# Optimization experiments

Hardware: AMD Instinct MI355X
Metric: run time of the kernel (lower is better)

Reference implementation:

```python
import jax, jax.numpy as jnp
import numpy as np

N_NODES = 50000
N_EDGES = 800000
NEG_SLOPE = 0.2


def _gat_conv(h, src, dst, W, al, ar, b, res, act):
    """DGL-style GATConv. h:[N,Fin], W:[Fin,H*D], al/ar:[H,D], b:[H*D].
    res: None | [N,H,D] residual value. Returns [N,H,D]."""
    N = h.shape[0]
    H, D = al.shape
    ft = (h @ W).reshape(N, H, D)                       # projected features
    el = jnp.einsum('nhd,hd->nh', ft, al)               # [N,H]
    er = jnp.einsum('nhd,hd->nh', ft, ar)               # [N,H]
    e = jax.nn.leaky_relu(el[src] + er[dst], NEG_SLOPE) # [E,H] edge logits
    # edge softmax over incoming edges of each dst node
    emax = jax.ops.segment_max(e, dst, num_segments=N)  # [N,H]
    emax = jnp.where(jnp.isfinite(emax), emax, 0.0)     # guard empty segments
    ex = jnp.exp(e - emax[dst])                         # [E,H]
    denom = jax.ops.segment_sum(ex, dst, num_segments=N)
    a = ex / denom[dst]                                 # [E,H] attention
    rst = jax.ops.segment_sum(ft[src] * a[..., None], dst, num_segments=N)  # [N,H,D]
    if res is not None:
        rst = rst + res
    rst = rst + b.reshape(1, H, D)
    if act is not None:
        rst = act(rst)
    return rst


def setup_inputs() -> dict:
    key = jax.random.key(0)
    ks = jax.random.split(key, 16)
    s = 0.1
    return {
        'x': jax.random.normal(ks[0], (N_NODES, 128), jnp.float32),
        'edge_src': jax.random.randint(ks[1], (N_EDGES,), 0, N_NODES, jnp.int32),
        'edge_dst': jax.random.randint(ks[2], (N_EDGES,), 0, N_NODES, jnp.int32),
        'W0': jax.random.normal(ks[3], (128, 128), jnp.float32) * s,
        'al0': jax.random.normal(ks[4], (2, 64), jnp.float32) * s,
        'ar0': jax.random.normal(ks[5], (2, 64), jnp.float32) * s,
        'b0': jnp.zeros((128,), jnp.float32),
        'W1': jax.random.normal(ks[6], (128, 128), jnp.float32) * s,
        'al1': jax.random.normal(ks[7], (2, 64), jnp.float32) * s,
        'ar1': jax.random.normal(ks[8], (2, 64), jnp.float32) * s,
        'b1': jnp.zeros((128,), jnp.float32),
        'W2': jax.random.normal(ks[9], (128, 194), jnp.float32) * s,
        'al2': jax.random.normal(ks[10], (2, 97), jnp.float32) * s,
        'ar2': jax.random.normal(ks[11], (2, 97), jnp.float32) * s,
        'b2': jnp.zeros((194,), jnp.float32),
        'res_W2': jax.random.normal(ks[12], (128, 194), jnp.float32) * s,
    }


def reference(x, edge_src, edge_dst, W0, al0, ar0, b0, W1, al1, ar1, b1,
              W2, al2, ar2, b2, res_W2):
    N = x.shape[0]
    elu = jax.nn.elu
    # layer 0: no residual, ELU
    h = _gat_conv(x, edge_src, edge_dst, W0, al0, ar0, b0, None, elu)
    h = h.reshape(N, -1)                                # flatten(1) -> [N,128]
    # layer 1: identity residual (in == heads*out), ELU
    res1 = h.reshape(N, 2, 64)
    h = _gat_conv(h, edge_src, edge_dst, W1, al1, ar1, b1, res1, elu)
    h = h.reshape(N, -1)
    # output layer: linear residual, no activation, mean over heads
    res2 = (h @ res_W2).reshape(N, 2, 97)
    logits = _gat_conv(h, edge_src, edge_dst, W2, al2, ar2, b2, res2, None)
    logits = logits.mean(axis=1)                        # [N, 97]
    # original slices off the last node of each graph (single batched graph)
    return logits[: N - 1]
```

## Files before the change

### kernel.cpp

```cpp
#include <hip/hip_runtime.h>
#include <math.h>

#define NNODES 50000
#define NEDGES 800000
#define NPAD   50048
#define NSLICE 8
#define SLICEN (NNODES / NSLICE)

typedef unsigned int uint;
typedef unsigned short u16;
typedef __bf16 bf16x8 __attribute__((ext_vector_type(8)));
typedef float f32x4 __attribute__((ext_vector_type(4)));

__device__ __forceinline__ float lrelu(float x){ return x > 0.f ? x : 0.2f*x; }
__device__ __forceinline__ float elu_f(float x){ return x > 0.f ? x : expm1f(x); }
__device__ __forceinline__ u16 f2bf(float f){
    uint u = __float_as_uint(f);
    return (u16)((u + 0x7fffu + ((u >> 16) & 1u)) >> 16);
}
__device__ __forceinline__ float bf2f(u16 h){ return __uint_as_float(((uint)h) << 16); }
__device__ __forceinline__ float blo(uint u){ return __uint_as_float(u << 16); }
__device__ __forceinline__ float bhi(uint u){ return __uint_as_float(u & 0xffff0000u); }

#define R0 (NPAD*32)
#define R1 (R0 + 256*128)
#define R2 (R1 + 128*384)
#define R3 (R2 + 256)
#define R4 (R3 + 128)
__global__ void prep_all(const float* __restrict__ x,
                         const float* __restrict__ W0, const float* __restrict__ W1,
                         const float* __restrict__ W2, const float* __restrict__ Wr,
                         const float* __restrict__ al2, const float* __restrict__ ar2,
                         const float* __restrict__ b2,
                         u16* __restrict__ Xb, u16* __restrict__ H1b,
                         u16* __restrict__ B01, u16* __restrict__ Bf,
                         float* __restrict__ alp2, float* __restrict__ arp2,
                         float* __restrict__ cb, int N)
{
    int idx = blockIdx.x * blockDim.x + threadIdx.x;
    if (idx < R0) {
        int n = idx >> 5;
        ushort4 hv = make_ushort4(0,0,0,0);
        if (n < N) {
            float4 v = ((const float4*)x)[idx];
            hv.x = f2bf(v.x); hv.y = f2bf(v.y); hv.z = f2bf(v.z); hv.w = f2bf(v.w);
        } else {
            ((ushort4*)H1b)[idx] = make_ushort4(0,0,0,0);
        }
        ((ushort4*)Xb)[idx] = hv;
    } else if (idx < R1) {
        int j = idx - R0, gcol = j >> 7, k = j & 127;
        float v = (gcol < 128) ? W0[k*128 + gcol] : W1[k*128 + (gcol - 128)];
        B01[j] = f2bf(v);
    } else if (idx < R2) {
        int j = idx - R1, c = j / 384, k = j - c*384;
        float v = 0.f;
        if (c < 97) {
            if (k < 128)      v = W2[k*194 + c];
            else if (k < 256) v = W2[(k-128)*194 + 97 + c];
            else              v = Wr[(k-256)*194 + c] + Wr[(k-256)*194 + 97 + c];
        }
        Bf[c*384 + k] = f2bf(v);
    } else if (idx < R3) {
        int t = idx - R2, k = t & 127, h = t >> 7;
        float sl = 0.f, sr = 0.f;
        for (int d = 0; d < 97; d++) {
            float w = W2[k*194 + h*97 + d];
            sl += w * al2[h*97 + d];
            sr += w * ar2[h*97 + d];
        }
        alp2[h*128 + k] = sl;
        arp2[h*128 + k] = sr;
    } else if (idx < R4) {
        int c = idx - R3;
        if (c < 97) cb[c] = 0.5f * (b2[c] + b2[97 + c]);
    }
}

__global__ __launch_bounds__(256, 4)
void gemm_l01(const u16* __restrict__ Ab, const u16* __restrict__ Bh, u16* __restrict__ obf,
              const float* __restrict__ alv, const float* __restrict__ arv,
              float* __restrict__ el, float* __restrict__ er, int N)
{
    __shared__ u16 sB[128 * 136];
    const int bm = blockIdx.x * 64;
    const int tid = threadIdx.x, wid = tid >> 6, lane = tid & 63;
    const int lr = lane & 15, q = lane >> 4, lk8 = q << 3;

    bf16x8 aH[4];
    {
        size_t abase = (size_t)(bm + wid*16 + lr) * 128 + lk8;
        #pragma unroll
        for (int kt = 0; kt < 4; kt++)
            aH[kt] = *(const bf16x8*)(Ab + abase + kt*32);
    }
    {
        const int c = tid >> 1, seg = (tid & 1) * 64;
        const u16* g = Bh + (size_t)c * 128 + seg;
        u16* s = sB + c * 136 + seg;
        #pragma unroll
        for (int j = 0; j < 8; j++)
            *(uint4*)(s + j*8) = *(const uint4*)(g + j*8);
    }
    __syncthreads();

    f32x4 acc[8];
    #pragma unroll
    for (int i = 0; i < 8; i++) acc[i] = (f32x4){0.f,0.f,0.f,0.f};

    #pragma unroll
    for (int kt = 0; kt < 4; kt++)
        #pragma unroll
        for (int fs = 0; fs < 8; fs++) {
            bf16x8 b = *(const bf16x8*)(sB + (fs*16 + lr)*136 + kt*32 + lk8);
            acc[fs] = __builtin_amdgcn_mfma_f32_16x16x32_bf16(aH[kt], b, acc[fs], 0, 0, 0);
        }

    float el0[4] = {0,0,0,0}, el1[4] = {0,0,0,0}, er0[4] = {0,0,0,0}, er1[4] = {0,0,0,0};
    #pragma unroll
    for (int fs = 0; fs < 8; fs++) {
        const int col = fs*16 + lr;
        const float av = alv[col], gv = arv[col];
        #pragma unroll
        for (int v = 0; v < 4; v++) {
            float f = acc[fs][v];
            int row = bm + wid*16 + q*4 + v;
            if (row < N) obf[(size_t)row * 128 + col] = f2bf(f);
            if (fs < 4) { el0[v] += f * av; er0[v] += f * gv; }
            else        { el1[v] += f * av; er1[v] += f * gv; }
        }
    }
    #pragma unroll
    for (int off = 1; off < 16; off <<= 1) {
        #pragma unroll
        for (int v = 0; v < 4; v++) {
            el0[v] += __shfl_xor(el0[v], off);
            el1[v] += __shfl_xor(el1[v], off);
            er0[v] += __shfl_xor(er0[v], off);
            er1[v] += __shfl_xor(er1[v], off);
        }
    }
    if (lr == 0) {
        #pragma unroll
        for (int v = 0; v < 4; v++) {
            int row = bm + wid*16 + q*4 + v;
            if (row < N) {
                *(float2*)(el + 2*(size_t)row) = make_float2(el0[v], el1[v]);
                *(float2*)(er + 2*(size_t)row) = make_float2(er0[v], er1[v]);
            }
        }
    }
}

__global__ __launch_bounds__(256, 3)
void gemm_final(const u16* __restrict__ agg01, const u16* __restrict__ h2b,
                const u16* __restrict__ Bf, const float* __restrict__ cb,
                float* __restrict__ out, int N)
{
    __shared__ u16 sB[64 * 392];
    const int bid = blockIdx.x;
    const int x = (bid >> 4) * 8 + (bid & 7);
    const int ct = (bid >> 3) & 1;
    if (x >= NPAD / 64) return;
    const int bm = x * 64;
    const int tid = threadIdx.x, wid = tid >> 6, lane = tid & 63;
    const int lr = lane & 15, q = lane >> 4, lk8 = q << 3;

    bf16x8 aF[12];
    {
        const int row = bm + wid*16 + lr;
        const u16* pa = agg01 + (size_t)row * 256;
        #pragma unroll
        for (int kt = 0; kt < 8; kt++)
            aF[kt] = *(const bf16x8*)(pa + kt*32 + lk8);
        const u16* ph = h2b + (size_t)row * 128;
        #pragma unroll
        for (int kt = 0; kt < 4; kt++)
            aF[8 + kt] = *(const bf16x8*)(ph + kt*32 + lk8);
    }
    {
        const int c = tid >> 2, seg = (tid & 3) * 96;
        const u16* g = Bf + (size_t)(ct*64 + c) * 384 + seg;
        u16* s = sB + c * 392 + seg;
        #pragma unroll
        for (int j = 0; j < 12; j++)
            *(uint4*)(s + j*8) = *(const uint4*)(g + j*8);
    }
    __syncthreads();

    f32x4 acc[4];
    #pragma unroll
    for (int i = 0; i < 4; i++) acc[i] = (f32x4){0.f,0.f,0.f,0.f};

    #pragma unroll
    for (int kt = 0; kt < 12; kt++)
        #pragma unroll
        for (int fs = 0; fs < 4; fs++) {
            bf16x8 b = *(const bf16x8*)(sB + (fs*16 + lr)*392 + kt*32 + lk8);
            acc[fs] = __builtin_amdgcn_mfma_f32_16x16x32_bf16(aF[kt], b, acc[fs], 0, 0, 0);
        }

    #pragma unroll
    for (int fs = 0; fs < 4; fs++) {
        const int col = ct*64 + fs*16 + lr;
        if (col >= 97) continue;
        const float cbc = cb[col];
        #pragma unroll
        for (int v = 0; v < 4; v++) {
            int row = bm + wid*16 + q*4 + v;
            if (row < N - 1) out[(size_t)row * 97 + col] = 0.5f * acc[fs][v] + cbc;
        }
    }
}

__global__ __launch_bounds__(256)
void hist_sliced(const int* __restrict__ dst, int* __restrict__ counts, int E)
{
    const int slice = blockIdx.x & (NSLICE - 1);
    const int lo = slice * SLICEN, hi = lo + SLICEN;
    const int stride = (gridDim.x >> 3) * blockDim.x;
    for (int i = (blockIdx.x >> 3) * blockDim.x + threadIdx.x; i < E; i += stride) {
        int d = dst[i];
        if (d >= lo && d < hi) atomicAdd(&counts[d], 1);
    }
}

__global__ __launch_bounds__(256)
void scatter_sliced(const int* __restrict__ src, const int* __restrict__ dst,
                    int* __restrict__ cursor, int* __restrict__ ssorted, int E)
{
    const int slice = blockIdx.x & (NSLICE - 1);
    const int lo = slice * SLICEN, hi = lo + SLICEN;
    const int stride = (gridDim.x >> 3) * blockDim.x;
    for (int i = (blockIdx.x >> 3) * blockDim.x + threadIdx.x; i < E; i += stride) {
        int d = dst[i];
        if (d >= lo && d < hi) {
            int p = atomicAdd(&cursor[d], 1);
            ssorted[p] = src[i];
        }
    }
}

__global__ __launch_bounds__(1024)
void scan_dl(int* __restrict__ cnt_cur, int* __restrict__ row_start,
             int* __restrict__ flags, int* __restrict__ prefixes, int n)
{
    __shared__ int wsum[16];
    __shared__ int sExc;
    const int tid = threadIdx.x, lane = tid & 63, wv = tid >> 6;
    const int i0 = blockIdx.x * 4096 + tid * 4;
    int c[4], v[4];
    #pragma unroll
    for (int j = 0; j < 4; j++) { int i = i0 + j; c[j] = (i < n) ? cnt_cur[i] : 0; }
    v[0] = c[0]; v[1] = v[0] + c[1]; v[2] = v[1] + c[2]; v[3] = v[2] + c[3];
    int t = v[3];
    #pragma unroll
    for (int off = 1; off < 64; off <<= 1) {
        int u = __shfl_up(t, off);
        if (lane >= off) t += u;
    }
    int texcl = t - v[3];
    if (lane == 63) wsum[wv] = t;
    __syncthreads();
    if (tid == 0) {
        int tot = 0;
        #pragma unroll
        for (int w = 0; w < 16; w++) tot += wsum[w];
        int exc = 0;
        if (blockIdx.x > 0) {
            while (atomicAdd(&flags[blockIdx.x - 1], 0) == 0) __builtin_amdgcn_s_sleep(2);
            exc = atomicAdd(&prefixes[blockIdx.x - 1], 0);
        } else {
            row_start[0] = 0;
        }
        atomicExch(&prefixes[blockIdx.x], exc + tot);
        __threadfence();
        atomicExch(&flags[blockIdx.x], 1);
        sExc = exc;
    }
    __syncthreads();
    int woff = sExc + texcl;
    for (int w = 0; w < 16; w++) if (w < wv) woff += wsum[w];
    #pragma unroll
    for (int j = 0; j < 4; j++) {
        int i = i0 + j;
        if (i < n) {
            int inc = woff + v[j];
            row_start[i + 1] = inc;
            cnt_cur[i] = inc - c[j];
        }
    }
}

template<int MODE>
__global__ __launch_bounds__(256)
void gat_agg128(const uint* __restrict__ ftb, const float* __restrict__ el,
                const float* __restrict__ er, const int* __restrict__ row_start,
                const int* __restrict__ ssorted, const u16* __restrict__ Rb,
                const float* __restrict__ bias, u16* __restrict__ Hb,
                const float* __restrict__ alp2, const float* __restrict__ arp2,
                float* __restrict__ el2, float* __restrict__ er2)
{
    __shared__ int   s_src[4][64];
    __shared__ float s_w[4][2][64];
    const int wv = threadIdx.x >> 6, lane = threadIdx.x & 63;
    const int n = blockIdx.x * 4 + wv;
    const int beg = row_start[n];
    const int deg = row_start[n+1] - beg;
    const float2 ern = *(const float2*)(er + 2*(size_t)n);
    const int h = lane >> 5;
    float ax = 0.f, ay = 0.f, dp0 = 0.f, dp1 = 0.f;

    for (int cb = 0; cb < deg; cb += 64) {
        const int cnt = min(64, deg - cb);
        float w0 = 0.f, w1 = 0.f; int s = 0;
        if (lane < cnt) {
            s = ssorted[beg + cb + lane];
            float2 e = *(const float2*)(el + 2*(size_t)s);
            w0 = __expf(lrelu(e.x + ern.x));
            w1 = __expf(lrelu(e.y + ern.y));
        }
        dp0 += w0; dp1 += w1;
        s_src[wv][lane] = s; s_w[wv][0][lane] = w0; s_w[wv][1][lane] = w1;
        asm volatile("s_waitcnt lgkmcnt(0)" ::: "memory");
        int t = 0;
        for (; t + 8 <= cnt; t += 8) {
            int4   sa = *(const int4*)&s_src[wv][t];
            int4   sb = *(const int4*)&s_src[wv][t+4];
            float4 wa = *(const float4*)&s_w[wv][h][t];
            float4 wb = *(const float4*)&s_w[wv][h][t+4];
            int   sv[8] = {sa.x,sa.y,sa.z,sa.w,sb.x,sb.y,sb.z,sb.w};
            float wj[8] = {wa.x,wa.y,wa.z,wa.w,wb.x,wb.y,wb.z,wb.w};
            uint U[8];
            #pragma unroll
            for (int j = 0; j < 8; j++) U[j] = ftb[((uint)sv[j] << 6) + lane];
            #pragma unroll
            for (int j = 0; j < 8; j++) { ax += wj[j]*blo(U[j]); ay += wj[j]*bhi(U[j]); }
        }
        for (; t < cnt; t++) {
            int sv = s_src[wv][t];
            float w = s_w[wv][h][t];
            uint u = ftb[((uint)sv << 6) + lane];
            ax += w*blo(u); ay += w*bhi(u);
        }
    }
    #pragma unroll
    for (int off = 32; off; off >>= 1) { dp0 += __shfl_xor(dp0, off); dp1 += __shfl_xor(dp1, off); }
    const float den = (h == 0) ? dp0 : dp1;
    float r0 = (deg > 0) ? ax / den : 0.f;
    float r1 = (deg > 0) ? ay / den : 0.f;
    const int c0 = 2 * lane;
    const size_t ob = (size_t)n*128 + c0;
    const float2 bv = *(const float2*)(bias + c0);
    float v0 = r0 + bv.x, v1 = r1 + bv.y;
    if (MODE == 1) {
        ushort2 rv = *(const ushort2*)&Rb[ob];
        v0 += bf2f(rv.x);
        v1 += bf2f(rv.y);
    }
    v0 = elu_f(v0); v1 = elu_f(v1);
    *(ushort2*)&Hb[ob] = make_ushort2(f2bf(v0), f2bf(v1));

    if constexpr (MODE == 1) {
        float2 a0 = *(const float2*)(alp2 + c0);
        float2 a1 = *(const float2*)(alp2 + 128 + c0);
        float2 g0 = *(const float2*)(arp2 + c0);
        float2 g1 = *(const float2*)(arp2 + 128 + c0);
        float e0 = v0*a0.x + v1*a0.y;
        float e1 = v0*a1.x + v1*a1.y;
        float f0 = v0*g0.x + v1*g0.y;
        float f1 = v0*g1.x + v1*g1.y;
        #pragma unroll
        for (int off = 32; off; off >>= 1) {
            e0 += __shfl_xor(e0, off); e1 += __shfl_xor(e1, off);
            f0 += __shfl_xor(f0, off); f1 += __shfl_xor(f1, off);
        }
        if (lane == 0) {
            *(float2*)(el2 + 2*(size_t)n) = make_float2(e0, e1);
            *(float2*)(er2 + 2*(size_t)n) = make_float2(f0, f1);
        }
    }
}

__global__ __launch_bounds__(256)
void gat_agg_out2(const uint* __restrict__ h2u, const float* __restrict__ el,
                  const float* __restrict__ er, const int* __restrict__ row_start,
                  const int* __restrict__ ssorted, u16* __restrict__ agg01)
{
    __shared__ int   s_src[4][64];
    __shared__ float s_w[4][2][64];
    const int wv = threadIdx.x >> 6, lane = threadIdx.x & 63;
    const int n = blockIdx.x * 4 + wv;
    const int beg = row_start[n];
    const int deg = row_start[n+1] - beg;
    const float2 ern = *(const float2*)(er + 2*(size_t)n);
    float ax0 = 0.f, ay0 = 0.f, ax1 = 0.f, ay1 = 0.f, dp0 = 0.f, dp1 = 0.f;

    for (int cb = 0; cb < deg; cb += 64) {
        const int cnt = min(64, deg - cb);
        float w0 = 0.f, w1 = 0.f; int s = 0;
        if (lane < cnt) {
            s = ssorted[beg + cb + lane];
            float2 e = *(const float2*)(el + 2*(size_t)s);
            w0 = __expf(lrelu(e.x + ern.x));
            w1 = __expf(lrelu(e.y + ern.y));
        }
        dp0 += w0; dp1 += w1;
        s_src[wv][lane] = s; s_w[wv][0][lane] = w0; s_w[wv][1][lane] = w1;
        asm volatile("s_waitcnt lgkmcnt(0)" ::: "memory");
        int t = 0;
        for (; t + 8 <= cnt; t += 8) {
            int4   sa = *(const int4*)&s_src[wv][t];
            int4   sb = *(const int4*)&s_src[wv][t+4];
            float4 p0a = *(const float4*)&s_w[wv][0][t];
            float4 p0b = *(const float4*)&s_w[wv][0][t+4];
            float4 p1a = *(const float4*)&s_w[wv][1][t];
            float4 p1b = *(const float4*)&s_w[wv][1][t+4];
            int   sv[8] = {sa.x,sa.y,sa.z,sa.w,sb.x,sb.y,sb.z,sb.w};
            float f0[8] = {p0a.x,p0a.y,p0a.z,p0a.w,p0b.x,p0b.y,p0b.z,p0b.w};
            float f1[8] = {p1a.x,p1a.y,p1a.z,p1a.w,p1b.x,p1b.y,p1b.z,p1b.w};
            uint U[8];
            #pragma unroll
            for (int j = 0; j < 8; j++) U[j] = h2u[((uint)sv[j] << 6) + lane];
            #pragma unroll
            for (int j = 0; j < 8; j++) {
                float lo = blo(U[j]), hi = bhi(U[j]);
                ax0 += f0[j]*lo; ay0 += f0[j]*hi;
                ax1 += f1[j]*lo; ay1 += f1[j]*hi;
            }
        }
        for (; t < cnt; t++) {
            int sv = s_src[wv][t];
            float f0 = s_w[wv][0][t], f1 = s_w[wv][1][t];
            uint u = h2u[((uint)sv << 6) + lane];
            float lo = blo(u), hi = bhi(u);
            ax0 += f0*lo; ay0 += f0*hi;
            ax1 += f1*lo; ay1 += f1*hi;
        }
    }
    #pragma unroll
    for (int off = 32; off; off >>= 1) { dp0 += __shfl_xor(dp0, off); dp1 += __shfl_xor(dp1, off); }
    const float i0 = (deg > 0) ? 1.f/dp0 : 0.f;
    const float i1 = (deg > 0) ? 1.f/dp1 : 0.f;
    const int c0 = 2 * lane;
    *(ushort2*)&agg01[(size_t)n*256 + c0]       = make_ushort2(f2bf(ax0*i0), f2bf(ay0*i0));
    *(ushort2*)&agg01[(size_t)n*256 + 128 + c0] = make_ushort2(f2bf(ax1*i1), f2bf(ay1*i1));
}

extern "C" void kernel_launch(void* const* d_in, const int* in_sizes, int n_in,
                              void* d_out, int out_size, void* d_ws, size_t ws_size,
                              hipStream_t stream)
{
    const float* x   = (const float*)d_in[0];
    const int*   esrc= (const int*)  d_in[1];
    const int*   edst= (const int*)  d_in[2];
    const float* W0  = (const float*)d_in[3];
    const float* al0 = (const float*)d_in[4];
    const float* ar0 = (const float*)d_in[5];
    const float* b0  = (const float*)d_in[6];
    const float* W1  = (const float*)d_in[7];
    const float* al1 = (const float*)d_in[8];
    const float* ar1 = (const float*)d_in[9];
    const float* b1  = (const float*)d_in[10];
    const float* W2  = (const float*)d_in[11];
    const float* al2 = (const float*)d_in[12];
    const float* ar2 = (const float*)d_in[13];
    const float* b2  = (const float*)d_in[14];
    const float* rW2 = (const float*)d_in[15];
    float* out = (float*)d_out;

    const int N = NNODES, E = NEDGES;
    const int NB = (N + 4095) / 4096;
    float* ws = (float*)d_ws;
    size_t o = 0;
    auto alloc_f = [&](size_t count) { float* p = ws + o; o += (count + 3) & ~(size_t)3; return p; };
    float* el    = alloc_f((size_t)N * 2);
    float* er    = alloc_f((size_t)N * 2);
    float* el2   = alloc_f((size_t)N * 2);
    float* er2   = alloc_f((size_t)N * 2);
    uint*  ftb   = (uint*)alloc_f((size_t)N * 64);
    u16*   agg01 = (u16*)alloc_f((size_t)NPAD * 128);
    u16*   Xb    = (u16*)alloc_f((size_t)NPAD * 64);
    u16*   H1b   = (u16*)alloc_f((size_t)NPAD * 64);
    u16*   B01   = (u16*)alloc_f(256 * 64);
    u16*   Bf    = (u16*)alloc_f(128 * 192);
    float* alp2  = alloc_f(256);
    float* arp2  = alloc_f(256);
    float* cbv   = alloc_f(128);
    int* row_start = (int*)alloc_f(N + 4);
    int* cursor    = (int*)alloc_f(N + 64);
    int* flags     = cursor + N;
    int* prefixes  = cursor + N + 16;
    int* ssorted   = (int*)alloc_f(E);

    hipMemsetAsync(cursor, 0, (N + 64) * sizeof(int), stream);
    hist_sliced<<<NSLICE * 256, 256, 0, stream>>>(edst, cursor, E);
    scan_dl<<<NB, 1024, 0, stream>>>(cursor, row_start, flags, prefixes, N);
    scatter_sliced<<<NSLICE * 256, 256, 0, stream>>>(esrc, edst, cursor, ssorted, E);

    prep_all<<<(R4 + 255) / 256, 256, 0, stream>>>(x, W0, W1, W2, rW2, al2, ar2, b2,
                                                   Xb, H1b, B01, Bf, alp2, arp2, cbv, N);

    const int gx = NPAD / 64;
    const int agg_grid = N / 4;

    gemm_l01<<<gx, 256, 0, stream>>>(Xb, B01, (u16*)ftb, al0, ar0, el, er, N);
    gat_agg128<0><<<agg_grid, 256, 0, stream>>>(ftb, el, er, row_start, ssorted,
                                                nullptr, b0, H1b, nullptr, nullptr, nullptr, nullptr);

    gemm_l01<<<gx, 256, 0, stream>>>(H1b, B01 + 128*128, (u16*)ftb, al1, ar1, el, er, N);
    gat_agg128<1><<<agg_grid, 256, 0, stream>>>(ftb, el, er, row_start, ssorted,
                                                H1b, b1, Xb, alp2, arp2, el2, er2);

    gat_agg_out2<<<agg_grid, 256, 0, stream>>>((uint*)Xb, el2, er2, row_start, ssorted, agg01);
    gemm_final<<<((gx + 7) / 8) * 16, 256, 0, stream>>>(agg01, Xb, Bf, cbv, out, N);
}
```

Baseline: 281.2 us.

## Vectorize GAT neighbor gathers with 16-byte loads and merge prep with histogram

```diff
diff --git a/kernel.cpp b/kernel.cpp
--- a/kernel.cpp
+++ b/kernel.cpp
@@ -27,17 +27,32 @@
 #define R2 (R1 + 128*384)
 #define R3 (R2 + 256)
 #define R4 (R3 + 128)
-__global__ void prep_all(const float* __restrict__ x,
-                         const float* __restrict__ W0, const float* __restrict__ W1,
-                         const float* __restrict__ W2, const float* __restrict__ Wr,
-                         const float* __restrict__ al2, const float* __restrict__ ar2,
-                         const float* __restrict__ b2,
-                         u16* __restrict__ Xb, u16* __restrict__ H1b,
-                         u16* __restrict__ B01, u16* __restrict__ Bf,
-                         float* __restrict__ alp2, float* __restrict__ arp2,
-                         float* __restrict__ cb, int N)
-{
-    int idx = blockIdx.x * blockDim.x + threadIdx.x;
+#define PREPB ((R4 + 255) / 256)
+#define HISTB 2048
+__global__ __launch_bounds__(256)
+void prep_hist(const float* __restrict__ x,
+               const float* __restrict__ W0, const float* __restrict__ W1,
+               const float* __restrict__ W2, const float* __restrict__ Wr,
+               const float* __restrict__ al2, const float* __restrict__ ar2,
+               const float* __restrict__ b2,
+               const int* __restrict__ edst, int* __restrict__ counts,
+               u16* __restrict__ Xb, u16* __restrict__ H1b,
+               u16* __restrict__ B01, u16* __restrict__ Bf,
+               float* __restrict__ alp2, float* __restrict__ arp2,
+               float* __restrict__ cb, int N)
+{
+    if (blockIdx.x >= PREPB) {
+        const int hb = blockIdx.x - PREPB;
+        const int slice = hb & (NSLICE - 1);
+        const int lo = slice * SLICEN, hi = lo + SLICEN;
+        const int stride = (HISTB >> 3) * 256;
+        for (int i = (hb >> 3) * 256 + (int)threadIdx.x; i < NEDGES; i += stride) {
+            int d = edst[i];
+            if (d >= lo && d < hi) atomicAdd(&counts[d], 1);
+        }
+        return;
+    }
+    int idx = blockIdx.x * 256 + threadIdx.x;
     if (idx < R0) {
         int n = idx >> 5;
         ushort4 hv = make_ushort4(0,0,0,0);
@@ -214,18 +229,6 @@
 }
 
 __global__ __launch_bounds__(256)
-void hist_sliced(const int* __restrict__ dst, int* __restrict__ counts, int E)
-{
-    const int slice = blockIdx.x & (NSLICE - 1);
-    const int lo = slice * SLICEN, hi = lo + SLICEN;
-    const int stride = (gridDim.x >> 3) * blockDim.x;
-    for (int i = (blockIdx.x >> 3) * blockDim.x + threadIdx.x; i < E; i += stride) {
-        int d = dst[i];
-        if (d >= lo && d < hi) atomicAdd(&counts[d], 1);
-    }
-}
-
-__global__ __launch_bounds__(256)
 void scatter_sliced(const int* __restrict__ src, const int* __restrict__ dst,
                     int* __restrict__ cursor, int* __restrict__ ssorted, int E)
 {
@@ -308,8 +311,11 @@
     const int beg = row_start[n];
     const int deg = row_start[n+1] - beg;
     const float2 ern = *(const float2*)(er + 2*(size_t)n);
-    const int h = lane >> 5;
-    float ax = 0.f, ay = 0.f, dp0 = 0.f, dp1 = 0.f;
+    const int eg = lane >> 4;
+    const int c4 = (lane & 15) << 2;
+    const int hh = (lane & 15) >> 3;
+    float acc[8] = {};
+    float dp0 = 0.f, dp1 = 0.f;
 
     for (int cb = 0; cb < deg; cb += 64) {
         const int cnt = min(64, deg - cb);
@@ -323,61 +329,72 @@
         dp0 += w0; dp1 += w1;
         s_src[wv][lane] = s; s_w[wv][0][lane] = w0; s_w[wv][1][lane] = w1;
         asm volatile("s_waitcnt lgkmcnt(0)" ::: "memory");
-        int t = 0;
-        for (; t + 8 <= cnt; t += 8) {
-            int4   sa = *(const int4*)&s_src[wv][t];
-            int4   sb = *(const int4*)&s_src[wv][t+4];
-            float4 wa = *(const float4*)&s_w[wv][h][t];
-            float4 wb = *(const float4*)&s_w[wv][h][t+4];
-            int   sv[8] = {sa.x,sa.y,sa.z,sa.w,sb.x,sb.y,sb.z,sb.w};
-            float wj[8] = {wa.x,wa.y,wa.z,wa.w,wb.x,wb.y,wb.z,wb.w};
-            uint U[8];
+        for (int e0 = 0; e0 < cnt; e0 += 16) {
+            uint4 U[4]; float w[4];
             #pragma unroll
-            for (int j = 0; j < 8; j++) U[j] = ftb[((uint)sv[j] << 6) + lane];
+            for (int j = 0; j < 4; j++) {
+                int e = e0 + j*4 + eg;
+                int sv = s_src[wv][e];
+                w[j] = s_w[wv][hh][e];
+                U[j] = *(const uint4*)(ftb + ((size_t)(uint)sv << 6) + c4);
+            }
             #pragma unroll
-            for (int j = 0; j < 8; j++) { ax += wj[j]*blo(U[j]); ay += wj[j]*bhi(U[j]); }
-        }
-        for (; t < cnt; t++) {
-            int sv = s_src[wv][t];
-            float w = s_w[wv][h][t];
-            uint u = ftb[((uint)sv << 6) + lane];
-            ax += w*blo(u); ay += w*bhi(u);
+            for (int j = 0; j < 4; j++) {
+                acc[0] += w[j]*blo(U[j].x); acc[1] += w[j]*bhi(U[j].x);
+                acc[2] += w[j]*blo(U[j].y); acc[3] += w[j]*bhi(U[j].y);
+                acc[4] += w[j]*blo(U[j].z); acc[5] += w[j]*bhi(U[j].z);
+                acc[6] += w[j]*blo(U[j].w); acc[7] += w[j]*bhi(U[j].w);
+            }
         }
     }
     #pragma unroll
     for (int off = 32; off; off >>= 1) { dp0 += __shfl_xor(dp0, off); dp1 += __shfl_xor(dp1, off); }
-    const float den = (h == 0) ? dp0 : dp1;
-    float r0 = (deg > 0) ? ax / den : 0.f;
-    float r1 = (deg > 0) ? ay / den : 0.f;
-    const int c0 = 2 * lane;
-    const size_t ob = (size_t)n*128 + c0;
-    const float2 bv = *(const float2*)(bias + c0);
-    float v0 = r0 + bv.x, v1 = r1 + bv.y;
-    if (MODE == 1) {
-        ushort2 rv = *(const ushort2*)&Rb[ob];
-        v0 += bf2f(rv.x);
-        v1 += bf2f(rv.y);
-    }
-    v0 = elu_f(v0); v1 = elu_f(v1);
-    *(ushort2*)&Hb[ob] = make_ushort2(f2bf(v0), f2bf(v1));
-
-    if constexpr (MODE == 1) {
-        float2 a0 = *(const float2*)(alp2 + c0);
-        float2 a1 = *(const float2*)(alp2 + 128 + c0);
-        float2 g0 = *(const float2*)(arp2 + c0);
-        float2 g1 = *(const float2*)(arp2 + 128 + c0);
-        float e0 = v0*a0.x + v1*a0.y;
-        float e1 = v0*a1.x + v1*a1.y;
-        float f0 = v0*g0.x + v1*g0.y;
-        float f1 = v0*g1.x + v1*g1.y;
-        #pragma unroll
-        for (int off = 32; off; off >>= 1) {
-            e0 += __shfl_xor(e0, off); e1 += __shfl_xor(e1, off);
-            f0 += __shfl_xor(f0, off); f1 += __shfl_xor(f1, off);
-        }
-        if (lane == 0) {
-            *(float2*)(el2 + 2*(size_t)n) = make_float2(e0, e1);
-            *(float2*)(er2 + 2*(size_t)n) = make_float2(f0, f1);
+    #pragma unroll
+    for (int k = 0; k < 8; k++) {
+        acc[k] += __shfl_xor(acc[k], 16);
+        acc[k] += __shfl_xor(acc[k], 32);
+    }
+    const float den = (hh == 0) ? dp0 : dp1;
+    const float inv = (deg > 0) ? 1.f / den : 0.f;
+    if (lane < 16) {
+        const int c0 = lane << 3;
+        float v[8];
+        float4 b0 = *(const float4*)(bias + c0);
+        float4 b1 = *(const float4*)(bias + c0 + 4);
+        v[0]=acc[0]*inv+b0.x; v[1]=acc[1]*inv+b0.y; v[2]=acc[2]*inv+b0.z; v[3]=acc[3]*inv+b0.w;
+        v[4]=acc[4]*inv+b1.x; v[5]=acc[5]*inv+b1.y; v[6]=acc[6]*inv+b1.z; v[7]=acc[7]*inv+b1.w;
+        if (MODE == 1) {
+            uint4 rv = *(const uint4*)(Rb + (size_t)n*128 + c0);
+            v[0]+=blo(rv.x); v[1]+=bhi(rv.x); v[2]+=blo(rv.y); v[3]+=bhi(rv.y);
+            v[4]+=blo(rv.z); v[5]+=bhi(rv.z); v[6]+=blo(rv.w); v[7]+=bhi(rv.w);
+        }
+        #pragma unroll
+        for (int k = 0; k < 8; k++) v[k] = elu_f(v[k]);
+        uint4 ov;
+        ov.x = (uint)f2bf(v[0]) | ((uint)f2bf(v[1]) << 16);
+        ov.y = (uint)f2bf(v[2]) | ((uint)f2bf(v[3]) << 16);
+        ov.z = (uint)f2bf(v[4]) | ((uint)f2bf(v[5]) << 16);
+        ov.w = (uint)f2bf(v[6]) | ((uint)f2bf(v[7]) << 16);
+        *(uint4*)(Hb + (size_t)n*128 + c0) = ov;
+        if (MODE == 1) {
+            float e0s=0.f, e1s=0.f, f0s=0.f, f1s=0.f;
+            #pragma unroll
+            for (int k = 0; k < 8; k++) {
+                float hv = v[k];
+                e0s += hv * alp2[c0 + k];
+                e1s += hv * alp2[128 + c0 + k];
+                f0s += hv * arp2[c0 + k];
+                f1s += hv * arp2[128 + c0 + k];
+            }
+            #pragma unroll
+            for (int off = 1; off < 16; off <<= 1) {
+                e0s += __shfl_xor(e0s, off); e1s += __shfl_xor(e1s, off);
+                f0s += __shfl_xor(f0s, off); f1s += __shfl_xor(f1s, off);
+            }
+            if (lane == 0) {
+                *(float2*)(el2 + 2*(size_t)n) = make_float2(e0s, e1s);
+                *(float2*)(er2 + 2*(size_t)n) = make_float2(f0s, f1s);
+            }
         }
     }
 }
@@ -394,7 +411,10 @@
     const int beg = row_start[n];
     const int deg = row_start[n+1] - beg;
     const float2 ern = *(const float2*)(er + 2*(size_t)n);
-    float ax0 = 0.f, ay0 = 0.f, ax1 = 0.f, ay1 = 0.f, dp0 = 0.f, dp1 = 0.f;
+    const int eg = lane >> 4;
+    const int c4 = (lane & 15) << 2;
+    float a0[8] = {}, a1[8] = {};
+    float dp0 = 0.f, dp1 = 0.f;
 
     for (int cb = 0; cb < deg; cb += 64) {
         const int cnt = min(64, deg - cb);
@@ -408,43 +428,53 @@
         dp0 += w0; dp1 += w1;
         s_src[wv][lane] = s; s_w[wv][0][lane] = w0; s_w[wv][1][lane] = w1;
         asm volatile("s_waitcnt lgkmcnt(0)" ::: "memory");
-        int t = 0;
-        for (; t + 8 <= cnt; t += 8) {
-            int4   sa = *(const int4*)&s_src[wv][t];
-            int4   sb = *(const int4*)&s_src[wv][t+4];
-            float4 p0a = *(const float4*)&s_w[wv][0][t];
-            float4 p0b = *(const float4*)&s_w[wv][0][t+4];
-            float4 p1a = *(const float4*)&s_w[wv][1][t];
-            float4 p1b = *(const float4*)&s_w[wv][1][t+4];
-            int   sv[8] = {sa.x,sa.y,sa.z,sa.w,sb.x,sb.y,sb.z,sb.w};
-            float f0[8] = {p0a.x,p0a.y,p0a.z,p0a.w,p0b.x,p0b.y,p0b.z,p0b.w};
-            float f1[8] = {p1a.x,p1a.y,p1a.z,p1a.w,p1b.x,p1b.y,p1b.z,p1b.w};
-            uint U[8];
+        for (int e0 = 0; e0 < cnt; e0 += 16) {
+            uint4 U[4]; float u0[4], u1[4];
             #pragma unroll
-            for (int j = 0; j < 8; j++) U[j] = h2u[((uint)sv[j] << 6) + lane];
+            for (int j = 0; j < 4; j++) {
+                int e = e0 + j*4 + eg;
+                int sv = s_src[wv][e];
+                u0[j] = s_w[wv][0][e];
+                u1[j] = s_w[wv][1][e];
+                U[j] = *(const uint4*)(h2u + ((size_t)(uint)sv << 6) + c4);
+            }
             #pragma unroll
-            for (int j = 0; j < 8; j++) {
-                float lo = blo(U[j]), hi = bhi(U[j]);
-                ax0 += f0[j]*lo; ay0 += f0[j]*hi;
-                ax1 += f1[j]*lo; ay1 += f1[j]*hi;
-            }
-        }
-        for (; t < cnt; t++) {
-            int sv = s_src[wv][t];
-            float f0 = s_w[wv][0][t], f1 = s_w[wv][1][t];
-            uint u = h2u[((uint)sv << 6) + lane];
-            float lo = blo(u), hi = bhi(u);
-            ax0 += f0*lo; ay0 += f0*hi;
-            ax1 += f1*lo; ay1 += f1*hi;
+            for (int j = 0; j < 4; j++) {
+                float lo, hi;
+                lo = blo(U[j].x); hi = bhi(U[j].x);
+                a0[0]+=u0[j]*lo; a1[0]+=u1[j]*lo; a0[1]+=u0[j]*hi; a1[1]+=u1[j]*hi;
+                lo = blo(U[j].y); hi = bhi(U[j].y);
+                a0[2]+=u0[j]*lo; a1[2]+=u1[j]*lo; a0[3]+=u0[j]*hi; a1[3]+=u1[j]*hi;
+                lo = blo(U[j].z); hi = bhi(U[j].z);
+                a0[4]+=u0[j]*lo; a1[4]+=u1[j]*lo; a0[5]+=u0[j]*hi; a1[5]+=u1[j]*hi;
+                lo = blo(U[j].w); hi = bhi(U[j].w);
+                a0[6]+=u0[j]*lo; a1[6]+=u1[j]*lo; a0[7]+=u0[j]*hi; a1[7]+=u1[j]*hi;
+            }
         }
     }
     #pragma unroll
     for (int off = 32; off; off >>= 1) { dp0 += __shfl_xor(dp0, off); dp1 += __shfl_xor(dp1, off); }
+    #pragma unroll
+    for (int k = 0; k < 8; k++) {
+        a0[k] += __shfl_xor(a0[k], 16); a0[k] += __shfl_xor(a0[k], 32);
+        a1[k] += __shfl_xor(a1[k], 16); a1[k] += __shfl_xor(a1[k], 32);
+    }
     const float i0 = (deg > 0) ? 1.f/dp0 : 0.f;
     const float i1 = (deg > 0) ? 1.f/dp1 : 0.f;
-    const int c0 = 2 * lane;
-    *(ushort2*)&agg01[(size_t)n*256 + c0]       = make_ushort2(f2bf(ax0*i0), f2bf(ay0*i0));
-    *(ushort2*)&agg01[(size_t)n*256 + 128 + c0] = make_ushort2(f2bf(ax1*i1), f2bf(ay1*i1));
+    if (lane < 16) {
+        const int c0 = lane << 3;
+        uint4 o0, o1;
+        o0.x = (uint)f2bf(a0[0]*i0) | ((uint)f2bf(a0[1]*i0) << 16);
+        o0.y = (uint)f2bf(a0[2]*i0) | ((uint)f2bf(a0[3]*i0) << 16);
+        o0.z = (uint)f2bf(a0[4]*i0) | ((uint)f2bf(a0[5]*i0) << 16);
+        o0.w = (uint)f2bf(a0[6]*i0) | ((uint)f2bf(a0[7]*i0) << 16);
+        o1.x = (uint)f2bf(a1[0]*i1) | ((uint)f2bf(a1[1]*i1) << 16);
+        o1.y = (uint)f2bf(a1[2]*i1) | ((uint)f2bf(a1[3]*i1) << 16);
+        o1.z = (uint)f2bf(a1[4]*i1) | ((uint)f2bf(a1[5]*i1) << 16);
+        o1.w = (uint)f2bf(a1[6]*i1) | ((uint)f2bf(a1[7]*i1) << 16);
+        *(uint4*)(agg01 + (size_t)n*256 + c0)       = o0;
+        *(uint4*)(agg01 + (size_t)n*256 + 128 + c0) = o1;
+    }
 }
 
 extern "C" void kernel_launch(void* const* d_in, const int* in_sizes, int n_in,
@@ -494,12 +524,11 @@
     int* ssorted   = (int*)alloc_f(E);
 
     hipMemsetAsync(cursor, 0, (N + 64) * sizeof(int), stream);
-    hist_sliced<<<NSLICE * 256, 256, 0, stream>>>(edst, cursor, E);
+    prep_hist<<<PREPB + HISTB, 256, 0, stream>>>(x, W0, W1, W2, rW2, al2, ar2, b2,
+                                                 edst, cursor,
+                                                 Xb, H1b, B01, Bf, alp2, arp2, cbv, N);
     scan_dl<<<NB, 1024, 0, stream>>>(cursor, row_start, flags, prefixes, N);
     scatter_sliced<<<NSLICE * 256, 256, 0, stream>>>(esrc, edst, cursor, ssorted, E);
-
-    prep_all<<<(R4 + 255) / 256, 256, 0, stream>>>(x, W0, W1, W2, rW2, al2, ar2, b2,
-                                                   Xb, H1b, B01, Bf, alp2, arp2, cbv, N);
 
     const int gx = NPAD / 64;
     const int agg_grid = N / 4;
```

New measurement: 285.5 us. Within noise of the previous version (+1.5%).

## Slice feature tensors by column and split edge softmax from sliced aggregation

Applied to the files above, without the earlier changes.

```diff
diff --git a/kernel.cpp b/kernel.cpp
--- a/kernel.cpp
+++ b/kernel.cpp
@@ -21,6 +21,8 @@
 __device__ __forceinline__ float bf2f(u16 h){ return __uint_as_float(((uint)h) << 16); }
 __device__ __forceinline__ float blo(uint u){ return __uint_as_float(u << 16); }
 __device__ __forceinline__ float bhi(uint u){ return __uint_as_float(u & 0xffff0000u); }
+__device__ __forceinline__ uint packbf(float a, float b){ return (uint)f2bf(a) | ((uint)f2bf(b) << 16); }
+
 
 #define R0 (NPAD*32)
 #define R1 (R0 + 256*128)
@@ -39,15 +41,17 @@
 {
     int idx = blockIdx.x * blockDim.x + threadIdx.x;
     if (idx < R0) {
-        int n = idx >> 5;
+        int n = idx >> 5, g = idx & 31;
+        int s = g >> 3, cu2 = (g & 7) * 2;
+        size_t off16 = (((size_t)s * NPAD + n) * 16 + cu2) * 2;
         ushort4 hv = make_ushort4(0,0,0,0);
         if (n < N) {
             float4 v = ((const float4*)x)[idx];
             hv.x = f2bf(v.x); hv.y = f2bf(v.y); hv.z = f2bf(v.z); hv.w = f2bf(v.w);
         } else {
-            ((ushort4*)H1b)[idx] = make_ushort4(0,0,0,0);
-        }
-        ((ushort4*)Xb)[idx] = hv;
+            *(ushort4*)(H1b + off16) = make_ushort4(0,0,0,0);
+        }
+        *(ushort4*)(Xb + off16) = hv;
     } else if (idx < R1) {
         int j = idx - R0, gcol = j >> 7, k = j & 127;
         float v = (gcol < 128) ? W0[k*128 + gcol] : W1[k*128 + (gcol - 128)];
@@ -89,10 +93,10 @@
 
     bf16x8 aH[4];
     {
-        size_t abase = (size_t)(bm + wid*16 + lr) * 128 + lk8;
+        const int row = bm + wid*16 + lr;
         #pragma unroll
         for (int kt = 0; kt < 4; kt++)
-            aH[kt] = *(const bf16x8*)(Ab + abase + kt*32);
+            aH[kt] = *(const bf16x8*)(Ab + (((size_t)kt * NPAD + row) * 16 + q*4) * 2);
     }
     {
         const int c = tid >> 1, seg = (tid & 1) * 64;
@@ -120,12 +124,14 @@
     #pragma unroll
     for (int fs = 0; fs < 8; fs++) {
         const int col = fs*16 + lr;
+        const int cs = col >> 5, ccu = (col >> 1) & 15, cpar = col & 1;
         const float av = alv[col], gv = arv[col];
         #pragma unroll
         for (int v = 0; v < 4; v++) {
             float f = acc[fs][v];
             int row = bm + wid*16 + q*4 + v;
-            if (row < N) obf[(size_t)row * 128 + col] = f2bf(f);
+            if (row < N)
+                obf[(((size_t)cs * NPAD + row) * 16 + ccu) * 2 + cpar] = f2bf(f);
             if (fs < 4) { el0[v] += f * av; er0[v] += f * gv; }
             else        { el1[v] += f * av; er1[v] += f * gv; }
         }
@@ -169,14 +175,15 @@
     bf16x8 aF[12];
     {
         const int row = bm + wid*16 + lr;
-        const u16* pa = agg01 + (size_t)row * 256;
-        #pragma unroll
-        for (int kt = 0; kt < 8; kt++)
-            aF[kt] = *(const bf16x8*)(pa + kt*32 + lk8);
-        const u16* ph = h2b + (size_t)row * 128;
         #pragma unroll
         for (int kt = 0; kt < 4; kt++)
-            aF[8 + kt] = *(const bf16x8*)(ph + kt*32 + lk8);
+            aF[kt] = *(const bf16x8*)(agg01 + ((((size_t)kt * NPAD + row) * 2 + 0) * 16 + q*4) * 2);
+        #pragma unroll
+        for (int kt = 4; kt < 8; kt++)
+            aF[kt] = *(const bf16x8*)(agg01 + ((((size_t)(kt-4) * NPAD + row) * 2 + 1) * 16 + q*4) * 2);
+        #pragma unroll
+        for (int kt = 8; kt < 12; kt++)
+            aF[kt] = *(const bf16x8*)(h2b + (((size_t)(kt-8) * NPAD + row) * 16 + q*4) * 2);
     }
     {
         const int c = tid >> 2, seg = (tid & 3) * 96;
@@ -292,159 +299,120 @@
     }
 }
 
-template<int MODE>
 __global__ __launch_bounds__(256)
-void gat_agg128(const uint* __restrict__ ftb, const float* __restrict__ el,
-                const float* __restrict__ er, const int* __restrict__ row_start,
-                const int* __restrict__ ssorted, const u16* __restrict__ Rb,
-                const float* __restrict__ bias, u16* __restrict__ Hb,
-                const float* __restrict__ alp2, const float* __restrict__ arp2,
-                float* __restrict__ el2, float* __restrict__ er2)
-{
-    __shared__ int   s_src[4][64];
-    __shared__ float s_w[4][2][64];
+void edge_weights(const float* __restrict__ el, const float* __restrict__ er,
+                  const int* __restrict__ row_start, const int* __restrict__ ssorted,
+                  uint* __restrict__ wbuf, float2* __restrict__ invd)
+{
     const int wv = threadIdx.x >> 6, lane = threadIdx.x & 63;
     const int n = blockIdx.x * 4 + wv;
     const int beg = row_start[n];
     const int deg = row_start[n+1] - beg;
     const float2 ern = *(const float2*)(er + 2*(size_t)n);
-    const int h = lane >> 5;
-    float ax = 0.f, ay = 0.f, dp0 = 0.f, dp1 = 0.f;
-
+    float dp0 = 0.f, dp1 = 0.f;
     for (int cb = 0; cb < deg; cb += 64) {
         const int cnt = min(64, deg - cb);
-        float w0 = 0.f, w1 = 0.f; int s = 0;
         if (lane < cnt) {
-            s = ssorted[beg + cb + lane];
+            int s = ssorted[beg + cb + lane];
             float2 e = *(const float2*)(el + 2*(size_t)s);
-            w0 = __expf(lrelu(e.x + ern.x));
-            w1 = __expf(lrelu(e.y + ern.y));
-        }
-        dp0 += w0; dp1 += w1;
-        s_src[wv][lane] = s; s_w[wv][0][lane] = w0; s_w[wv][1][lane] = w1;
-        asm volatile("s_waitcnt lgkmcnt(0)" ::: "memory");
-        int t = 0;
-        for (; t + 8 <= cnt; t += 8) {
-            int4   sa = *(const int4*)&s_src[wv][t];
-            int4   sb = *(const int4*)&s_src[wv][t+4];
-            float4 wa = *(const float4*)&s_w[wv][h][t];
-            float4 wb = *(const float4*)&s_w[wv][h][t+4];
-            int   sv[8] = {sa.x,sa.y,sa.z,sa.w,sb.x,sb.y,sb.z,sb.w};
-            float wj[8] = {wa.x,wa.y,wa.z,wa.w,wb.x,wb.y,wb.z,wb.w};
-            uint U[8];
-            #pragma unroll
-            for (int j = 0; j < 8; j++) U[j] = ftb[((uint)sv[j] << 6) + lane];
-            #pragma unroll
-            for (int j = 0; j < 8; j++) { ax += wj[j]*blo(U[j]); ay += wj[j]*bhi(U[j]); }
-        }
-        for (; t < cnt; t++) {
-            int sv = s_src[wv][t];
-            float w = s_w[wv][h][t];
-            uint u = ftb[((uint)sv << 6) + lane];
-            ax += w*blo(u); ay += w*bhi(u);
+            float w0 = __expf(lrelu(e.x + ern.x));
+            float w1 = __expf(lrelu(e.y + ern.y));
+            dp0 += w0; dp1 += w1;
+            wbuf[beg + cb + lane] = packbf(w0, w1);
         }
     }
     #pragma unroll
     for (int off = 32; off; off >>= 1) { dp0 += __shfl_xor(dp0, off); dp1 += __shfl_xor(dp1, off); }
-    const float den = (h == 0) ? dp0 : dp1;
-    float r0 = (deg > 0) ? ax / den : 0.f;
-    float r1 = (deg > 0) ? ay / den : 0.f;
-    const int c0 = 2 * lane;
-    const size_t ob = (size_t)n*128 + c0;
-    const float2 bv = *(const float2*)(bias + c0);
-    float v0 = r0 + bv.x, v1 = r1 + bv.y;
-    if (MODE == 1) {
-        ushort2 rv = *(const ushort2*)&Rb[ob];
-        v0 += bf2f(rv.x);
-        v1 += bf2f(rv.y);
-    }
-    v0 = elu_f(v0); v1 = elu_f(v1);
-    *(ushort2*)&Hb[ob] = make_ushort2(f2bf(v0), f2bf(v1));
-
-    if constexpr (MODE == 1) {
-        float2 a0 = *(const float2*)(alp2 + c0);
-        float2 a1 = *(const float2*)(alp2 + 128 + c0);
-        float2 g0 = *(const float2*)(arp2 + c0);
-        float2 g1 = *(const float2*)(arp2 + 128 + c0);
-        float e0 = v0*a0.x + v1*a0.y;
-        float e1 = v0*a1.x + v1*a1.y;
-        float f0 = v0*g0.x + v1*g0.y;
-        float f1 = v0*g1.x + v1*g1.y;
-        #pragma unroll
-        for (int off = 32; off; off >>= 1) {
-            e0 += __shfl_xor(e0, off); e1 += __shfl_xor(e1, off);
-            f0 += __shfl_xor(f0, off); f1 += __shfl_xor(f1, off);
-        }
-        if (lane == 0) {
-            *(float2*)(el2 + 2*(size_t)n) = make_float2(e0, e1);
-            *(float2*)(er2 + 2*(size_t)n) = make_float2(f0, f1);
-        }
-    }
-}
-
+    if (lane == 0)
+        invd[n] = (deg > 0) ? make_float2(1.f/dp0, 1.f/dp1) : make_float2(0.f, 0.f);
+}
+
+template<int MODE>
 __global__ __launch_bounds__(256)
-void gat_agg_out2(const uint* __restrict__ h2u, const float* __restrict__ el,
-                  const float* __restrict__ er, const int* __restrict__ row_start,
-                  const int* __restrict__ ssorted, u16* __restrict__ agg01)
-{
-    __shared__ int   s_src[4][64];
-    __shared__ float s_w[4][2][64];
+void sagg(const uint* __restrict__ T, const int* __restrict__ row_start,
+          const int* __restrict__ ssorted, const uint* __restrict__ wbuf,
+          const float2* __restrict__ invd, const float* __restrict__ bias,
+          const uint* __restrict__ Tres, uint* __restrict__ Tout)
+{
+    const int wv = threadIdx.x >> 6, lane = threadIdx.x & 63;
+    const int b7 = blockIdx.x & 7;
+    const int slice = b7 >> 1;
+    const int n = ((blockIdx.x >> 3) * 2 + (b7 & 1)) * 4 + wv;
+    const int cu = lane & 15, eg = lane >> 4;
+    const int beg = row_start[n];
+    const int deg = row_start[n+1] - beg;
+    const uint* __restrict__ Ts = T + (size_t)slice * NPAD * 16;
+    float al = 0.f, ah = 0.f, bl = 0.f, bh = 0.f;
+
+    for (int e0 = 0; e0 < deg; e0 += 4) {
+        const int e = e0 + eg;
+        const bool valid = (e < deg);
+        const int idx = beg + e;
+        const int s = valid ? ssorted[idx] : 0;
+        const uint wp = valid ? wbuf[idx] : 0u;
+        const uint U = Ts[(size_t)(uint)s * 16 + cu];
+        const float w0 = blo(wp), w1 = bhi(wp);
+        if constexpr (MODE < 2) {
+            const float w = (slice < 2) ? w0 : w1;
+            al += w * blo(U); ah += w * bhi(U);
+        } else {
+            const float lo = blo(U), hi = bhi(U);
+            al += w0 * lo; ah += w0 * hi;
+            bl += w1 * lo; bh += w1 * hi;
+        }
+    }
+    al += __shfl_xor(al, 16); al += __shfl_xor(al, 32);
+    ah += __shfl_xor(ah, 16); ah += __shfl_xor(ah, 32);
+    if constexpr (MODE == 2) {
+        bl += __shfl_xor(bl, 16); bl += __shfl_xor(bl, 32);
+        bh += __shfl_xor(bh, 16); bh += __shfl_xor(bh, 32);
+    }
+    if (lane < 16) {
+        const float2 iv = invd[n];
+        if constexpr (MODE < 2) {
+            const float inv = (slice < 2) ? iv.x : iv.y;
+            const int col0 = slice*32 + 2*lane;
+            float v0 = al * inv + bias[col0];
+            float v1 = ah * inv + bias[col0 + 1];
+            if constexpr (MODE == 1) {
+                uint r = Tres[((size_t)slice * NPAD + n) * 16 + lane];
+                v0 += blo(r); v1 += bhi(r);
+            }
+            v0 = elu_f(v0); v1 = elu_f(v1);
+            Tout[((size_t)slice * NPAD + n) * 16 + lane] = packbf(v0, v1);
+        } else {
+            const size_t b = ((size_t)slice * NPAD + n) * 32 + lane;
+            Tout[b]      = packbf(al * iv.x, ah * iv.x);
+            Tout[b + 16] = packbf(bl * iv.y, bh * iv.y);
+        }
+    }
+}
+
+__global__ __launch_bounds__(256)
+void elr2_kernel(const uint* __restrict__ Th2, const float* __restrict__ alp2,
+                 const float* __restrict__ arp2, float* __restrict__ el2,
+                 float* __restrict__ er2, int N)
+{
     const int wv = threadIdx.x >> 6, lane = threadIdx.x & 63;
     const int n = blockIdx.x * 4 + wv;
-    const int beg = row_start[n];
-    const int deg = row_start[n+1] - beg;
-    const float2 ern = *(const float2*)(er + 2*(size_t)n);
-    float ax0 = 0.f, ay0 = 0.f, ax1 = 0.f, ay1 = 0.f, dp0 = 0.f, dp1 = 0.f;
-
-    for (int cb = 0; cb < deg; cb += 64) {
-        const int cnt = min(64, deg - cb);
-        float w0 = 0.f, w1 = 0.f; int s = 0;
-        if (lane < cnt) {
-            s = ssorted[beg + cb + lane];
-            float2 e = *(const float2*)(el + 2*(size_t)s);
-            w0 = __expf(lrelu(e.x + ern.x));
-            w1 = __expf(lrelu(e.y + ern.y));
-        }
-        dp0 += w0; dp1 += w1;
-        s_src[wv][lane] = s; s_w[wv][0][lane] = w0; s_w[wv][1][lane] = w1;
-        asm volatile("s_waitcnt lgkmcnt(0)" ::: "memory");
-        int t = 0;
-        for (; t + 8 <= cnt; t += 8) {
-            int4   sa = *(const int4*)&s_src[wv][t];
-            int4   sb = *(const int4*)&s_src[wv][t+4];
-            float4 p0a = *(const float4*)&s_w[wv][0][t];
-            float4 p0b = *(const float4*)&s_w[wv][0][t+4];
-            float4 p1a = *(const float4*)&s_w[wv][1][t];
-            float4 p1b = *(const float4*)&s_w[wv][1][t+4];
-            int   sv[8] = {sa.x,sa.y,sa.z,sa.w,sb.x,sb.y,sb.z,sb.w};
-            float f0[8] = {p0a.x,p0a.y,p0a.z,p0a.w,p0b.x,p0b.y,p0b.z,p0b.w};
-            float f1[8] = {p1a.x,p1a.y,p1a.z,p1a.w,p1b.x,p1b.y,p1b.z,p1b.w};
-            uint U[8];
-            #pragma unroll
-            for (int j = 0; j < 8; j++) U[j] = h2u[((uint)sv[j] << 6) + lane];
-            #pragma unroll
-            for (int j = 0; j < 8; j++) {
-                float lo = blo(U[j]), hi = bhi(U[j]);
-                ax0 += f0[j]*lo; ay0 += f0[j]*hi;
-                ax1 += f1[j]*lo; ay1 += f1[j]*hi;
-            }
-        }
-        for (; t < cnt; t++) {
-            int sv = s_src[wv][t];
-            float f0 = s_w[wv][0][t], f1 = s_w[wv][1][t];
-            uint u = h2u[((uint)sv << 6) + lane];
-            float lo = blo(u), hi = bhi(u);
-            ax0 += f0*lo; ay0 += f0*hi;
-            ax1 += f1*lo; ay1 += f1*hi;
-        }
-    }
-    #pragma unroll
-    for (int off = 32; off; off >>= 1) { dp0 += __shfl_xor(dp0, off); dp1 += __shfl_xor(dp1, off); }
-    const float i0 = (deg > 0) ? 1.f/dp0 : 0.f;
-    const float i1 = (deg > 0) ? 1.f/dp1 : 0.f;
-    const int c0 = 2 * lane;
-    *(ushort2*)&agg01[(size_t)n*256 + c0]       = make_ushort2(f2bf(ax0*i0), f2bf(ay0*i0));
-    *(ushort2*)&agg01[(size_t)n*256 + 128 + c0] = make_ushort2(f2bf(ax1*i1), f2bf(ay1*i1));
+    if (n >= N) return;
+    const int s = lane >> 4, cu = lane & 15;
+    const uint u = Th2[((size_t)s * NPAD + n) * 16 + cu];
+    const int c0 = s*32 + 2*cu;
+    const float f0 = blo(u), f1 = bhi(u);
+    float e0 = f0*alp2[c0]     + f1*alp2[c0+1];
+    float e1 = f0*alp2[128+c0] + f1*alp2[129+c0];
+    float r0 = f0*arp2[c0]     + f1*arp2[c0+1];
+    float r1 = f0*arp2[128+c0] + f1*arp2[129+c0];
+    #pragma unroll
+    for (int off = 32; off; off >>= 1) {
+        e0 += __shfl_xor(e0, off); e1 += __shfl_xor(e1, off);
+        r0 += __shfl_xor(r0, off); r1 += __shfl_xor(r1, off);
+    }
+    if (lane == 0) {
+        *(float2*)(el2 + 2*(size_t)n) = make_float2(e0, e1);
+        *(float2*)(er2 + 2*(size_t)n) = make_float2(r0, r1);
+    }
 }
 
 extern "C" void kernel_launch(void* const* d_in, const int* in_sizes, int n_in,
@@ -474,24 +442,26 @@
     float* ws = (float*)d_ws;
     size_t o = 0;
     auto alloc_f = [&](size_t count) { float* p = ws + o; o += (count + 3) & ~(size_t)3; return p; };
-    float* el    = alloc_f((size_t)N * 2);
-    float* er    = alloc_f((size_t)N * 2);
-    float* el2   = alloc_f((size_t)N * 2);
-    float* er2   = alloc_f((size_t)N * 2);
-    uint*  ftb   = (uint*)alloc_f((size_t)N * 64);
-    u16*   agg01 = (u16*)alloc_f((size_t)NPAD * 128);
-    u16*   Xb    = (u16*)alloc_f((size_t)NPAD * 64);
-    u16*   H1b   = (u16*)alloc_f((size_t)NPAD * 64);
-    u16*   B01   = (u16*)alloc_f(256 * 64);
-    u16*   Bf    = (u16*)alloc_f(128 * 192);
-    float* alp2  = alloc_f(256);
-    float* arp2  = alloc_f(256);
-    float* cbv   = alloc_f(128);
+    float*  el    = alloc_f((size_t)N * 2);
+    float*  er    = alloc_f((size_t)N * 2);
+    float*  el2   = alloc_f((size_t)N * 2);
+    float*  er2   = alloc_f((size_t)N * 2);
+    float2* invd  = (float2*)alloc_f((size_t)N * 2);
+    uint*   wbuf  = (uint*)alloc_f((size_t)E);
+    uint*   ftb   = (uint*)alloc_f((size_t)NPAD * 64);
+    uint*   Th1   = (uint*)alloc_f((size_t)NPAD * 64);
+    uint*   Tx    = (uint*)alloc_f((size_t)NPAD * 64);
+    uint*   TA    = (uint*)alloc_f((size_t)NPAD * 128);
+    u16*    B01   = (u16*)alloc_f(256 * 64);
+    u16*    Bf    = (u16*)alloc_f(128 * 192);
+    float*  alp2  = alloc_f(256);
+    float*  arp2  = alloc_f(256);
+    float*  cbv   = alloc_f(128);
     int* row_start = (int*)alloc_f(N + 4);
     int* cursor    = (int*)alloc_f(N + 64);
     int* flags     = cursor + N;
     int* prefixes  = cursor + N + 16;
-    int* ssorted   = (int*)alloc_f(E);
+    int* ssorted   = (int*)alloc_f(E + 8);
 
     hipMemsetAsync(cursor, 0, (N + 64) * sizeof(int), stream);
     hist_sliced<<<NSLICE * 256, 256, 0, stream>>>(edst, cursor, E);
@@ -499,19 +469,22 @@
     scatter_sliced<<<NSLICE * 256, 256, 0, stream>>>(esrc, edst, cursor, ssorted, E);
 
     prep_all<<<(R4 + 255) / 256, 256, 0, stream>>>(x, W0, W1, W2, rW2, al2, ar2, b2,
-                                                   Xb, H1b, B01, Bf, alp2, arp2, cbv, N);
+                                                   (u16*)Tx, (u16*)Th1, B01, Bf, alp2, arp2, cbv, N);
 
     const int gx = NPAD / 64;
-    const int agg_grid = N / 4;
-
-    gemm_l01<<<gx, 256, 0, stream>>>(Xb, B01, (u16*)ftb, al0, ar0, el, er, N);
-    gat_agg128<0><<<agg_grid, 256, 0, stream>>>(ftb, el, er, row_start, ssorted,
-                                                nullptr, b0, H1b, nullptr, nullptr, nullptr, nullptr);
-
-    gemm_l01<<<gx, 256, 0, stream>>>(H1b, B01 + 128*128, (u16*)ftb, al1, ar1, el, er, N);
-    gat_agg128<1><<<agg_grid, 256, 0, stream>>>(ftb, el, er, row_start, ssorted,
-                                                H1b, b1, Xb, alp2, arp2, el2, er2);
-
-    gat_agg_out2<<<agg_grid, 256, 0, stream>>>((uint*)Xb, el2, er2, row_start, ssorted, agg01);
-    gemm_final<<<((gx + 7) / 8) * 16, 256, 0, stream>>>(agg01, Xb, Bf, cbv, out, N);
-}
+    const int node_grid = N / 4;
+    const int sagg_grid = (N / 4) * 4;
+
+    gemm_l01<<<gx, 256, 0, stream>>>((u16*)Tx, B01, (u16*)ftb, al0, ar0, el, er, N);
+    edge_weights<<<node_grid, 256, 0, stream>>>(el, er, row_start, ssorted, wbuf, invd);
+    sagg<0><<<sagg_grid, 256, 0, stream>>>(ftb, row_start, ssorted, wbuf, invd, b0, nullptr, Th1);
+
+    gemm_l01<<<gx, 256, 0, stream>>>((u16*)Th1, B01 + 128*128, (u16*)ftb, al1, ar1, el, er, N);
+    edge_weights<<<node_grid, 256, 0, stream>>>(el, er, row_start, ssorted, wbuf, invd);
+    sagg<1><<<sagg_grid, 256, 0, stream>>>(ftb, row_start, ssorted, wbuf, invd, b1, Th1, Tx);
+
+    elr2_kernel<<<node_grid, 256, 0, stream>>>(Tx, alp2, arp2, el2, er2, N);
+    edge_weights<<<node_grid, 256, 0, stream>>>(el2, er2, row_start, ssorted, wbuf, invd);
+    sagg<2><<<sagg_grid, 256, 0, stream>>>(Tx, row_start, ssorted, wbuf, invd, b0, nullptr, TA);
+    gemm_final<<<((gx + 7) / 8) * 16, 256, 0, stream>>>((u16*)TA, (u16*)Tx, Bf, cbv, out, N);
+}
```

Result: slower. 537.9 us (+91.3%).
